# Performance work log

Hardware: AMD Instinct MI355X
Metric: run time of the kernel (lower is better)

Reference implementation:

```python
import jax, jax.numpy as jnp
import numpy as np

N, E = 50000, 800000
IN, H, OUT = 500, 128, 64


def _gcn_layer(x, src, dst, norm, W, b):
    # Linear transform first (PyG GCNConv applies lin before propagate)
    h = x @ W                                   # [N, F_out]
    msg = norm[:, None] * h[src]                # [E', F_out] gather
    out = jax.ops.segment_sum(msg, dst, num_segments=N)  # scatter-add
    return out + b


def setup_inputs() -> dict:
    key = jax.random.key(0)
    k = jax.random.split(key, 6)
    x = jax.random.normal(k[0], (N, IN), jnp.float32)
    edge_index = jax.random.randint(k[1], (2, E), 0, N, dtype=jnp.int32)
    # Glorot-style init like PyG GCNConv
    W1 = jax.random.normal(k[2], (IN, H), jnp.float32) * (1.0 / np.sqrt(IN))
    b1 = jnp.zeros((H,), jnp.float32)
    W2 = jax.random.normal(k[3], (H, OUT), jnp.float32) * (1.0 / np.sqrt(H))
    b2 = jnp.zeros((OUT,), jnp.float32)
    return {"x": x, "edge_index": edge_index, "W1": W1, "b1": b1, "W2": W2, "b2": b2}


def reference(x, edge_index, W1, b1, W2, b2):
    # Add self loops (PyG GCNConv default add_self_loops=True)
    loops = jnp.arange(N, dtype=edge_index.dtype)
    src = jnp.concatenate([edge_index[0], loops])
    dst = jnp.concatenate([edge_index[1], loops])
    # Symmetric degree normalization: deg computed on targets (col)
    deg = jax.ops.segment_sum(jnp.ones_like(src, dtype=x.dtype), dst, num_segments=N)
    dis = jnp.where(deg > 0, jax.lax.rsqrt(jnp.maximum(deg, 1.0)), 0.0)
    norm = dis[src] * dis[dst]                  # [E+N]
    h = jax.nn.relu(_gcn_layer(x, src, dst, norm, W1, b1))
    return _gcn_layer(h, src, dst, norm, W2, b2)
```

## Files before the change

### kernel.cpp

```cpp
#include <hip/hip_runtime.h>
#include <hip/hip_bf16.h>


typedef __attribute__((ext_vector_type(4))) float f32x4;
typedef __attribute__((ext_vector_type(8))) short short8;

static __device__ __forceinline__ unsigned short f2bf(float f) {
    unsigned int u = __float_as_uint(f);
    u += 0x7FFF + ((u >> 16) & 1);
    return (unsigned short)(u >> 16);
}
static __device__ __forceinline__ float bf2f(unsigned short h) {
    return __uint_as_float(((unsigned int)h) << 16);
}

static __device__ __forceinline__ void glds16(const void* g, void* l) {
    __builtin_amdgcn_global_load_lds(
        (const __attribute__((address_space(1))) void*)g,
        (__attribute__((address_space(3))) void*)l, 16, 0, 0);
}

__global__ void deg_accum_i(const int* __restrict__ dst, int* __restrict__ deg, int E) {
    int i = blockIdx.x * blockDim.x + threadIdx.x;
    if (i < E) atomicAdd(&deg[dst[i]], 1);
}

__global__ void prep_imgs(const float* __restrict__ W1, const float* __restrict__ W2,
                          unsigned short* __restrict__ I1, unsigned short* __restrict__ I2,
                          int* __restrict__ deg, int Nn) {
    int idx = blockIdx.x * 256 + threadIdx.x;
    if (idx < Nn) deg[idx] = 0;
    const int total1 = 16 * 1024;
    if (idx < total1) {
        int kt = idx >> 10, pl = (idx >> 9) & 1, slot = (idx >> 7) & 3, col = idx & 127;
        int k0 = kt * 32 + slot * 8;
#pragma unroll
        for (int j = 0; j < 8; j++) {
            int k = k0 + j;
            float v = (k < 500) ? W1[(size_t)k * 128 + col] : 0.f;
            unsigned short h = f2bf(v);
            I1[(size_t)idx * 8 + j] = pl ? f2bf(v - bf2f(h)) : h;
        }
    } else if (idx < total1 + 2048) {
        int i2 = idx - total1;
        int kt = i2 >> 9, pl = (i2 >> 8) & 1, slot = (i2 >> 6) & 3, col = i2 & 63;
        int k0 = kt * 32 + slot * 8;
#pragma unroll
        for (int j = 0; j < 8; j++) {
            float v = W2[(size_t)(k0 + j) * 64 + col];
            unsigned short h = f2bf(v);
            I2[(size_t)i2 * 8 + j] = pl ? f2bf(v - bf2f(h)) : h;
        }
    }
}

__global__ void scan_part(const int* __restrict__ deg, int* __restrict__ bsum, int N) {
    int tid = threadIdx.x, lane = tid & 63, wid = tid >> 6;
    int i = blockIdx.x * 256 + tid;
    int v = (i < N) ? deg[i] : 0;
#pragma unroll
    for (int off = 1; off < 64; off <<= 1) v += __shfl_xor(v, off, 64);
    __shared__ int ws[4];
    if (lane == 0) ws[wid] = v;
    __syncthreads();
    if (tid == 0) bsum[blockIdx.x] = ws[0] + ws[1] + ws[2] + ws[3];
}

__global__ __launch_bounds__(1024) void scan_top(const int* __restrict__ bsum, int nb,
                                                 int* __restrict__ boff, int* __restrict__ rp, int N) {
    __shared__ int wsum[16];
    int tid = threadIdx.x, lane = tid & 63, wid = tid >> 6;
    int v = (tid < nb) ? bsum[tid] : 0;
    int x = v;
#pragma unroll
    for (int off = 1; off < 64; off <<= 1) {
        int t = __shfl_up(x, off, 64);
        if (lane >= off) x += t;
    }
    if (lane == 63) wsum[wid] = x;
    __syncthreads();
    if (tid < 16) {
        int y = wsum[tid];
#pragma unroll
        for (int off = 1; off < 16; off <<= 1) {
            int t = __shfl_up(y, off, 16);
            if (tid >= off) y += t;
        }
        wsum[tid] = y;
    }
    __syncthreads();
    int base = wid ? wsum[wid - 1] : 0;
    if (tid < nb) boff[tid] = base + x - v;
    if (tid == 0) rp[N] = wsum[15];
}

__global__ void scan_final(int* __restrict__ deg, const int* __restrict__ boff,
                           int* __restrict__ rp, int* __restrict__ cursor, int N) {
    int tid = threadIdx.x, lane = tid & 63, wid = tid >> 6;
    int i = blockIdx.x * 256 + tid;
    int v = (i < N) ? deg[i] : 0;
    int x = v;
#pragma unroll
    for (int off = 1; off < 64; off <<= 1) {
        int t = __shfl_up(x, off, 64);
        if (lane >= off) x += t;
    }
    __shared__ int wsum[4];
    if (lane == 63) wsum[wid] = x;
    __syncthreads();
    int base = boff[blockIdx.x];
    for (int ww = 0; ww < wid; ww++) base += wsum[ww];
    int ex = base + x - v;
    if (i < N) {
        rp[i] = ex;
        cursor[i] = ex;
        ((float*)deg)[i] = rsqrtf((float)(v + 1));
    }
}

__global__ void csr_fill(const int* __restrict__ src, const int* __restrict__ dst,
                         int* __restrict__ cursor, int* __restrict__ csr_src, int E) {
    int e = blockIdx.x * blockDim.x + threadIdx.x;
    if (e < E) {
        int pos = atomicAdd(&cursor[dst[e]], 1);
        csr_src[pos] = src[e];
    }
}

template<int BN, int KT, int KFULL>
__global__ __launch_bounds__(256) void gemm_glds(
    const float* __restrict__ A, const unsigned char* __restrict__ Wimg,
    unsigned short* __restrict__ C, int M, int K) {
    constexpr int ABYTES = 64 * 32 * 4;
    constexpr int BBYTES = BN * 32 * 2 * 2;
    constexpr int STEP = ABYTES + BBYTES;
    constexpr int AINST = ABYTES / 1024;
    constexpr int BINST = BBYTES / 1024;
    constexpr int IPW = (AINST + BINST) / 4;
    constexpr int BIPW = BINST / 4;
    constexpr int NF = BN / 32;

    __shared__ unsigned char smem[2][STEP];

    const int tid = threadIdx.x, lane = tid & 63, w = tid >> 6;
    const int lrow = lane & 15, lq = lane >> 4;
    const int wrow = (w >> 1) * 32;
    const int wcol = (w & 1) * (BN / 2);
    const int bm = blockIdx.x * 64;

    f32x4 acc[2][NF] = {};

    float pr[8];
    if constexpr (KFULL < KT) {
        const int prow = tid >> 2, pk = (tid & 3) * 8;
        const int grow = bm + prow;
#pragma unroll
        for (int j = 0; j < 8; j++) {
            int k = KFULL * 32 + pk + j;
            pr[j] = (grow < M && k < K) ? A[(size_t)grow * K + k] : 0.f;
        }
    }

    auto STAGE = [&](int kt, int buf) {
        unsigned char* base = &smem[buf][0];
#pragma unroll
        for (int j = 0; j < IPW; j++) {
            int g = w * IPW + j;
            if (g < AINST) {
                int srow = bm + lane; if (srow >= M) srow = M - 1;
                glds16(A + (size_t)srow * K + kt * 32 + g * 4, base + g * 1024);
            } else {
                int b = g - AINST;
                glds16(Wimg + (size_t)kt * BBYTES + (size_t)b * 1024 + lane * 16,
                       base + ABYTES + b * 1024);
            }
        }
    };
    auto STAGE_B = [&](int kt, int buf) {
        unsigned char* base = &smem[buf][0];
#pragma unroll
        for (int j = 0; j < BIPW; j++) {
            int b = w * BIPW + j;
            glds16(Wimg + (size_t)kt * BBYTES + (size_t)b * 1024 + lane * 16,
                   base + ABYTES + b * 1024);
        }
    };
    auto REGWRITE = [&](int buf) {
        const int prow = tid >> 2, pk = (tid & 3) * 8;
        unsigned char* base = &smem[buf][0];
        int s0 = pk >> 2;
        *(float4*)(base + s0 * 1024 + prow * 16) = make_float4(pr[0], pr[1], pr[2], pr[3]);
        *(float4*)(base + (s0 + 1) * 1024 + prow * 16) = make_float4(pr[4], pr[5], pr[6], pr[7]);
    };
    auto COMPUTE = [&](int buf) {
        const unsigned char* base = &smem[buf][0];
        short8 ah[2], al[2];
#pragma unroll
        for (int m = 0; m < 2; m++) {
            int r = wrow + m * 16 + lrow;
            float4 f0 = *(const float4*)(base + (lq * 2) * 1024 + r * 16);
            float4 f1 = *(const float4*)(base + (lq * 2 + 1) * 1024 + r * 16);
            float fv[8] = {f0.x, f0.y, f0.z, f0.w, f1.x, f1.y, f1.z, f1.w};
#pragma unroll
            for (int e = 0; e < 8; e++) {
                unsigned short hu = f2bf(fv[e]);
                ah[m][e] = (short)hu;
                al[m][e] = (short)f2bf(fv[e] - bf2f(hu));
            }
        }
        short8 bh[NF], bl[NF];
#pragma unroll
        for (int n = 0; n < NF; n++) {
            int c = wcol + n * 16 + lrow;
            bh[n] = *(const short8*)(base + ABYTES + lq * (BN * 16) + c * 16);
            bl[n] = *(const short8*)(base + ABYTES + BBYTES / 2 + lq * (BN * 16) + c * 16);
        }
#pragma unroll
        for (int m = 0; m < 2; m++)
#pragma unroll
            for (int n = 0; n < NF; n++) {
                acc[m][n] = __builtin_amdgcn_mfma_f32_16x16x32_bf16(ah[m], bh[n], acc[m][n], 0, 0, 0);
                acc[m][n] = __builtin_amdgcn_mfma_f32_16x16x32_bf16(al[m], bh[n], acc[m][n], 0, 0, 0);
                acc[m][n] = __builtin_amdgcn_mfma_f32_16x16x32_bf16(ah[m], bl[n], acc[m][n], 0, 0, 0);
            }
    };

    STAGE(0, 0);
    __syncthreads();
    int cur = 0;
    for (int kt = 0; kt < KT; kt++) {
        if (kt + 1 < KT) {
            if constexpr (KFULL < KT) {
                if (kt + 1 == KFULL) { STAGE_B(kt + 1, cur ^ 1); REGWRITE(cur ^ 1); }
                else STAGE(kt + 1, cur ^ 1);
            } else {
                STAGE(kt + 1, cur ^ 1);
            }
        }
        COMPUTE(cur);
        __syncthreads();
        cur ^= 1;
    }

#pragma unroll
    for (int m = 0; m < 2; m++)
#pragma unroll
        for (int n = 0; n < NF; n++)
#pragma unroll
            for (int q = 0; q < 4; q++) {
                int row = bm + wrow + m * 16 + (lane >> 4) * 4 + q;
                int col = wcol + n * 16 + (lane & 15);
                if (row < M) C[(size_t)row * BN + col] = f2bf(acc[m][n][q]);
            }
}

__global__ __launch_bounds__(256) void gather128(
    const int* __restrict__ rp, const int* __restrict__ csr,
    const float* __restrict__ dis, const unsigned short* __restrict__ h,
    const float* __restrict__ bias, float* __restrict__ out, int Nn) {
    int n = (blockIdx.x * 256 + threadIdx.x) >> 6;
    int lane = threadIdx.x & 63;
    if (n >= Nn) return;
    const int hh = lane >> 5;
    const int l = lane & 31;
    int beg = rp[n], end = rp[n + 1];
    float4 a0 = {0,0,0,0}, a1 = {0,0,0,0}, a2 = {0,0,0,0}, a3 = {0,0,0,0};
    auto P = [&](int e, float4& a) {
        int s = csr[e];
        float w = dis[s];
        ushort4 v = *(const ushort4*)&h[(size_t)s * 128 + l * 4];
        a.x = fmaf(w, bf2f(v.x), a.x); a.y = fmaf(w, bf2f(v.y), a.y);
        a.z = fmaf(w, bf2f(v.z), a.z); a.w = fmaf(w, bf2f(v.w), a.w);
    };
    int j = beg + hh;
    for (; j + 6 < end; j += 8) { P(j, a0); P(j + 2, a1); P(j + 4, a2); P(j + 6, a3); }
    for (; j < end; j += 2) P(j, a0);
    float4 acc;
    acc.x = (a0.x + a1.x) + (a2.x + a3.x);
    acc.y = (a0.y + a1.y) + (a2.y + a3.y);
    acc.z = (a0.z + a1.z) + (a2.z + a3.z);
    acc.w = (a0.w + a1.w) + (a2.w + a3.w);
    acc.x += __shfl_xor(acc.x, 32);
    acc.y += __shfl_xor(acc.y, 32);
    acc.z += __shfl_xor(acc.z, 32);
    acc.w += __shfl_xor(acc.w, 32);
    float dn = dis[n];
    ushort4 hv = *(const ushort4*)&h[(size_t)n * 128 + l * 4];
    float4 b4 = *(const float4*)&bias[l * 4];
    float4 o;
    o.x = fmaxf(dn * (acc.x + dn * bf2f(hv.x)) + b4.x, 0.f);
    o.y = fmaxf(dn * (acc.y + dn * bf2f(hv.y)) + b4.y, 0.f);
    o.z = fmaxf(dn * (acc.z + dn * bf2f(hv.z)) + b4.z, 0.f);
    o.w = fmaxf(dn * (acc.w + dn * bf2f(hv.w)) + b4.w, 0.f);
    if (hh == 0) *(float4*)&out[(size_t)n * 128 + l * 4] = o;
}

__global__ __launch_bounds__(256) void gather64(
    const int* __restrict__ rp, const int* __restrict__ csr,
    const float* __restrict__ dis, const unsigned short* __restrict__ h,
    const float* __restrict__ bias, float* __restrict__ out, int Nn) {
    int n = (blockIdx.x * 256 + threadIdx.x) >> 6;
    int lane = threadIdx.x & 63;
    if (n >= Nn) return;
    const int q = lane >> 4;
    const int l = lane & 15;
    int beg = rp[n], end = rp[n + 1];
    float4 a0 = {0,0,0,0}, a1 = {0,0,0,0};
    auto P = [&](int e, float4& a) {
        int s = csr[e];
        float w = dis[s];
        ushort4 v = *(const ushort4*)&h[(size_t)s * 64 + l * 4];
        a.x = fmaf(w, bf2f(v.x), a.x); a.y = fmaf(w, bf2f(v.y), a.y);
        a.z = fmaf(w, bf2f(v.z), a.z); a.w = fmaf(w, bf2f(v.w), a.w);
    };
    int j = beg + q;
    for (; j + 4 < end; j += 8) { P(j, a0); P(j + 4, a1); }
    for (; j < end; j += 4) P(j, a0);
    float4 acc;
    acc.x = a0.x + a1.x; acc.y = a0.y + a1.y;
    acc.z = a0.z + a1.z; acc.w = a0.w + a1.w;
    acc.x += __shfl_xor(acc.x, 16); acc.x += __shfl_xor(acc.x, 32);
    acc.y += __shfl_xor(acc.y, 16); acc.y += __shfl_xor(acc.y, 32);
    acc.z += __shfl_xor(acc.z, 16); acc.z += __shfl_xor(acc.z, 32);
    acc.w += __shfl_xor(acc.w, 16); acc.w += __shfl_xor(acc.w, 32);
    float dn = dis[n];
    ushort4 hv = *(const ushort4*)&h[(size_t)n * 64 + l * 4];
    float4 b4 = *(const float4*)&bias[l * 4];
    float4 o;
    o.x = dn * (acc.x + dn * bf2f(hv.x)) + b4.x;
    o.y = dn * (acc.y + dn * bf2f(hv.y)) + b4.y;
    o.z = dn * (acc.z + dn * bf2f(hv.z)) + b4.z;
    o.w = dn * (acc.w + dn * bf2f(hv.w)) + b4.w;
    if (q == 0) *(float4*)&out[(size_t)n * 64 + l * 4] = o;
}

extern "C" void kernel_launch(void* const* d_in, const int* in_sizes, int n_in,
                              void* d_out, int out_size, void* d_ws, size_t ws_size,
                              hipStream_t stream) {
    const float* x  = (const float*)d_in[0];
    const int*   ei = (const int*)d_in[1];
    const float* W1 = (const float*)d_in[2];
    const float* b1 = (const float*)d_in[3];
    const float* W2 = (const float*)d_in[4];
    const float* b2 = (const float*)d_in[5];

    const int IN = 500, H = 128, OUT = 64;
    const int Nn = in_sizes[0] / IN;
    const int E  = in_sizes[1] / 2;
    const int* src  = ei;
    const int* dstp = ei + E;

    const int Npad = ((Nn + 63) / 64) * 64;
    const int nb   = (Nn + 255) / 256;

    int*   degdis  = (int*)d_ws;
    int*   rp      = degdis + Npad;
    int*   bsum    = rp + Npad + 64;
    int*   boff    = bsum + 1024;
    int*   cursor  = boff + 1024;
    int*   csr_src = cursor + Npad;
    unsigned short* I1 = (unsigned short*)(csr_src + ((E + 63) / 64) * 64);
    unsigned short* I2 = I1 + 16 * 8192;
    unsigned short* h1u = I2 + 4 * 4096;
    float* agg1    = (float*)(h1u + (size_t)Npad * H);
    unsigned short* h2u = h1u;
    float* dis     = (float*)degdis;
    float* out     = (float*)d_out;

    prep_imgs<<<(Nn + 255) / 256, 256, 0, stream>>>(W1, W2, I1, I2, degdis, Nn);
    deg_accum_i<<<(E + 255) / 256, 256, 0, stream>>>(dstp, degdis, E);
    scan_part<<<nb, 256, 0, stream>>>(degdis, bsum, Nn);
    scan_top<<<1, 1024, 0, stream>>>(bsum, nb, boff, rp, Nn);
    scan_final<<<nb, 256, 0, stream>>>(degdis, boff, rp, cursor, Nn);
    csr_fill<<<(E + 255) / 256, 256, 0, stream>>>(src, dstp, cursor, csr_src, E);

    gemm_glds<128, 16, 15><<<(Nn + 63) / 64, 256, 0, stream>>>(
        x, (const unsigned char*)I1, h1u, Nn, IN);
    gather128<<<(Nn + 3) / 4, 256, 0, stream>>>(rp, csr_src, dis, h1u, b1, agg1, Nn);

    gemm_glds<64, 4, 4><<<(Nn + 63) / 64, 256, 0, stream>>>(
        agg1, (const unsigned char*)I2, h2u, Nn, H);
    gather64<<<(Nn + 3) / 4, 256, 0, stream>>>(rp, csr_src, dis, h2u, b2, out, Nn);
}
```

Baseline: 217.1 us.

## Fuse CSR fill into first GEMM launch and change warp tiling

Merges the CSR-fill scatter kernel into the first-layer GEMM launch. Blocks are interleaved so one in every five runs a GEMM tile and the other four scatter edges, letting the memory-bound x@W1 GEMM overlap the atomic-heavy CSR build and saving one kernel launch. The GEMM body also changes warp tiling: each wave now computes 16 rows by the full BN columns instead of 32 rows by BN/2. This reuses each wave's A fragment across more B columns but reloads all of B per wave. The fused kernel's CSR blocks reserve the GEMM's shared memory without using it, which could limit occupancy.

```diff
diff --git a/kernel.cpp b/kernel.cpp
--- a/kernel.cpp
+++ b/kernel.cpp
@@ -118,37 +118,25 @@
     }
 }
 
-__global__ void csr_fill(const int* __restrict__ src, const int* __restrict__ dst,
-                         int* __restrict__ cursor, int* __restrict__ csr_src, int E) {
-    int e = blockIdx.x * blockDim.x + threadIdx.x;
-    if (e < E) {
-        int pos = atomicAdd(&cursor[dst[e]], 1);
-        csr_src[pos] = src[e];
-    }
-}
-
 template<int BN, int KT, int KFULL>
-__global__ __launch_bounds__(256) void gemm_glds(
+__device__ __forceinline__ void gemm_body(
+    int bid, unsigned char* sm,
     const float* __restrict__ A, const unsigned char* __restrict__ Wimg,
     unsigned short* __restrict__ C, int M, int K) {
     constexpr int ABYTES = 64 * 32 * 4;
-    constexpr int BBYTES = BN * 32 * 2 * 2;
+    constexpr int BBYTES = BN * 128;
     constexpr int STEP = ABYTES + BBYTES;
     constexpr int AINST = ABYTES / 1024;
     constexpr int BINST = BBYTES / 1024;
     constexpr int IPW = (AINST + BINST) / 4;
     constexpr int BIPW = BINST / 4;
-    constexpr int NF = BN / 32;
-
-    __shared__ unsigned char smem[2][STEP];
+    constexpr int NF = BN / 16;
 
     const int tid = threadIdx.x, lane = tid & 63, w = tid >> 6;
     const int lrow = lane & 15, lq = lane >> 4;
-    const int wrow = (w >> 1) * 32;
-    const int wcol = (w & 1) * (BN / 2);
-    const int bm = blockIdx.x * 64;
-
-    f32x4 acc[2][NF] = {};
+    const int bm = bid * 64;
+
+    f32x4 acc[NF] = {};
 
     float pr[8];
     if constexpr (KFULL < KT) {
@@ -162,7 +150,7 @@
     }
 
     auto STAGE = [&](int kt, int buf) {
-        unsigned char* base = &smem[buf][0];
+        unsigned char* base = sm + buf * STEP;
 #pragma unroll
         for (int j = 0; j < IPW; j++) {
             int g = w * IPW + j;
@@ -177,7 +165,7 @@
         }
     };
     auto STAGE_B = [&](int kt, int buf) {
-        unsigned char* base = &smem[buf][0];
+        unsigned char* base = sm + buf * STEP;
 #pragma unroll
         for (int j = 0; j < BIPW; j++) {
             int b = w * BIPW + j;
@@ -187,42 +175,39 @@
     };
     auto REGWRITE = [&](int buf) {
         const int prow = tid >> 2, pk = (tid & 3) * 8;
-        unsigned char* base = &smem[buf][0];
+        unsigned char* base = sm + buf * STEP;
         int s0 = pk >> 2;
         *(float4*)(base + s0 * 1024 + prow * 16) = make_float4(pr[0], pr[1], pr[2], pr[3]);
         *(float4*)(base + (s0 + 1) * 1024 + prow * 16) = make_float4(pr[4], pr[5], pr[6], pr[7]);
     };
     auto COMPUTE = [&](int buf) {
-        const unsigned char* base = &smem[buf][0];
-        short8 ah[2], al[2];
-#pragma unroll
-        for (int m = 0; m < 2; m++) {
-            int r = wrow + m * 16 + lrow;
+        const unsigned char* base = sm + buf * STEP;
+        short8 ah, al;
+        {
+            int r = w * 16 + lrow;
             float4 f0 = *(const float4*)(base + (lq * 2) * 1024 + r * 16);
             float4 f1 = *(const float4*)(base + (lq * 2 + 1) * 1024 + r * 16);
             float fv[8] = {f0.x, f0.y, f0.z, f0.w, f1.x, f1.y, f1.z, f1.w};
 #pragma unroll
             for (int e = 0; e < 8; e++) {
                 unsigned short hu = f2bf(fv[e]);
-                ah[m][e] = (short)hu;
-                al[m][e] = (short)f2bf(fv[e] - bf2f(hu));
+                ah[e] = (short)hu;
+                al[e] = (short)f2bf(fv[e] - bf2f(hu));
             }
         }
         short8 bh[NF], bl[NF];
 #pragma unroll
         for (int n = 0; n < NF; n++) {
-            int c = wcol + n * 16 + lrow;
+            int c = n * 16 + lrow;
             bh[n] = *(const short8*)(base + ABYTES + lq * (BN * 16) + c * 16);
             bl[n] = *(const short8*)(base + ABYTES + BBYTES / 2 + lq * (BN * 16) + c * 16);
         }
 #pragma unroll
-        for (int m = 0; m < 2; m++)
-#pragma unroll
-            for (int n = 0; n < NF; n++) {
-                acc[m][n] = __builtin_amdgcn_mfma_f32_16x16x32_bf16(ah[m], bh[n], acc[m][n], 0, 0, 0);
-                acc[m][n] = __builtin_amdgcn_mfma_f32_16x16x32_bf16(al[m], bh[n], acc[m][n], 0, 0, 0);
-                acc[m][n] = __builtin_amdgcn_mfma_f32_16x16x32_bf16(ah[m], bl[n], acc[m][n], 0, 0, 0);
-            }
+        for (int n = 0; n < NF; n++) {
+            acc[n] = __builtin_amdgcn_mfma_f32_16x16x32_bf16(ah, bh[n], acc[n], 0, 0, 0);
+            acc[n] = __builtin_amdgcn_mfma_f32_16x16x32_bf16(al, bh[n], acc[n], 0, 0, 0);
+            acc[n] = __builtin_amdgcn_mfma_f32_16x16x32_bf16(ah, bl[n], acc[n], 0, 0, 0);
+        }
     };
 
     STAGE(0, 0);
@@ -243,15 +228,46 @@
     }
 
 #pragma unroll
-    for (int m = 0; m < 2; m++)
-#pragma unroll
-        for (int n = 0; n < NF; n++)
-#pragma unroll
-            for (int q = 0; q < 4; q++) {
-                int row = bm + wrow + m * 16 + (lane >> 4) * 4 + q;
-                int col = wcol + n * 16 + (lane & 15);
-                if (row < M) C[(size_t)row * BN + col] = f2bf(acc[m][n][q]);
+    for (int n = 0; n < NF; n++)
+#pragma unroll
+        for (int q = 0; q < 4; q++) {
+            int row = bm + w * 16 + (lane >> 4) * 4 + q;
+            int col = n * 16 + (lane & 15);
+            if (row < M) C[(size_t)row * BN + col] = f2bf(acc[n][q]);
+        }
+}
+
+template<int BN, int KT, int KFULL>
+__global__ __launch_bounds__(256) void gemm_glds(
+    const float* __restrict__ A, const unsigned char* __restrict__ Wimg,
+    unsigned short* __restrict__ C, int M, int K) {
+    __shared__ unsigned char sm[2 * (8192 + BN * 128)];
+    gemm_body<BN, KT, KFULL>(blockIdx.x, sm, A, Wimg, C, M, K);
+}
+
+template<int BN, int KT, int KFULL>
+__global__ __launch_bounds__(256) void fat_gemm_csr(
+    const float* __restrict__ A, const unsigned char* __restrict__ Wimg,
+    unsigned short* __restrict__ C, int M, int K,
+    const int* __restrict__ src, const int* __restrict__ dst,
+    int* __restrict__ cursor, int* __restrict__ csr_src, int E,
+    int ngemm, int ncsr) {
+    __shared__ unsigned char sm[2 * (8192 + BN * 128)];
+    const int bid = blockIdx.x;
+    const int stripe = bid / 5, pos = bid % 5;
+    if (pos == 0) {
+        if (stripe < ngemm)
+            gemm_body<BN, KT, KFULL>(stripe, sm, A, Wimg, C, M, K);
+    } else {
+        int c = stripe * 4 + pos - 1;
+        if (c < ncsr) {
+            int e = c * 256 + threadIdx.x;
+            if (e < E) {
+                int p = atomicAdd(&cursor[dst[e]], 1);
+                csr_src[p] = src[e];
             }
+        }
+    }
 }
 
 __global__ __launch_bounds__(256) void gather128(
@@ -352,6 +368,8 @@
 
     const int Npad = ((Nn + 63) / 64) * 64;
     const int nb   = (Nn + 255) / 256;
+    const int ngemm = (Nn + 63) / 64;
+    const int ncsr  = (E + 255) / 256;
 
     int*   degdis  = (int*)d_ws;
     int*   rp      = degdis + Npad;
@@ -368,17 +386,18 @@
     float* out     = (float*)d_out;
 
     prep_imgs<<<(Nn + 255) / 256, 256, 0, stream>>>(W1, W2, I1, I2, degdis, Nn);
-    deg_accum_i<<<(E + 255) / 256, 256, 0, stream>>>(dstp, degdis, E);
+    deg_accum_i<<<ncsr, 256, 0, stream>>>(dstp, degdis, E);
     scan_part<<<nb, 256, 0, stream>>>(degdis, bsum, Nn);
     scan_top<<<1, 1024, 0, stream>>>(bsum, nb, boff, rp, Nn);
     scan_final<<<nb, 256, 0, stream>>>(degdis, boff, rp, cursor, Nn);
-    csr_fill<<<(E + 255) / 256, 256, 0, stream>>>(src, dstp, cursor, csr_src, E);
-
-    gemm_glds<128, 16, 15><<<(Nn + 63) / 64, 256, 0, stream>>>(
-        x, (const unsigned char*)I1, h1u, Nn, IN);
+
+    fat_gemm_csr<128, 16, 15><<<ngemm * 5, 256, 0, stream>>>(
+        x, (const unsigned char*)I1, h1u, Nn, IN,
+        src, dstp, cursor, csr_src, E, ngemm, ncsr);
+
     gather128<<<(Nn + 3) / 4, 256, 0, stream>>>(rp, csr_src, dis, h1u, b1, agg1, Nn);
 
-    gemm_glds<64, 4, 4><<<(Nn + 63) / 64, 256, 0, stream>>>(
+    gemm_glds<64, 4, 4><<<ngemm, 256, 0, stream>>>(
         agg1, (const unsigned char*)I2, h2u, Nn, H);
     gather64<<<(Nn + 3) / 4, 256, 0, stream>>>(rp, csr_src, dis, h2u, b2, out, Nn);
 }
```

Measured after the change: 185.6 us. -14.5%, faster.
